# Kernel tuning notes

Hardware: AMD Instinct MI355X
Metric: run time of the kernel (lower is better)

Reference implementation:

```python
import jax, jax.numpy as jnp
import numpy as np

N_HEADS = 8
HEAD_DIM = 64  # hidden_dim 512 / 8 heads
EPS = 1e-12    # F.normalize clamp_min eps


def setup_inputs() -> dict:
    key = jax.random.key(0)
    k1, k2, k3, k4 = jax.random.split(key, 4)
    B, C, H, W = 2, 256, 48, 48
    hidden = N_HEADS * HEAD_DIM
    x = jax.random.normal(k1, (B, C, H, W), dtype=jnp.float32)
    w_qkv = jax.random.normal(k2, (hidden * 3, C), dtype=jnp.float32) * 0.02
    w_proj = jax.random.normal(k3, (C, hidden), dtype=jnp.float32) * 0.02
    b_proj = jax.random.normal(k4, (C,), dtype=jnp.float32) * 0.02
    return {"x": x, "w_qkv": w_qkv, "w_proj": w_proj, "b_proj": b_proj}


def _l2norm_tokens(t):
    # normalize along the token axis (last dim), matching F.normalize(dim=-1)
    n = jnp.sqrt(jnp.sum(t * t, axis=-1, keepdims=True))
    return t / jnp.maximum(n, EPS)


def reference(x, w_qkv, w_proj, b_proj):
    B, C, H, W = x.shape
    N = H * W
    # 1x1 conv == channel matmul
    qkv = jnp.einsum('oc,bchw->bohw', w_qkv, x)  # [B, 3*hidden, H, W]
    qkv = qkv.reshape(B, 3, N_HEADS, HEAD_DIM, N)
    q, k, v = qkv[:, 0], qkv[:, 1], qkv[:, 2]    # each [B, h, d, N]
    q = _l2norm_tokens(q)
    k = _l2norm_tokens(k)
    # attn = q^T @ k over head_dim -> [B, h, N, N]; note: qk_scale unused in source
    attn = jnp.einsum('bhdn,bhdm->bhnm', q, k)
    attn = jax.nn.softmax(attn, axis=-1)
    # out = attn @ v^T -> [B, h, N, d], then permute to [B, h, d, N]
    out = jnp.einsum('bhnm,bhdm->bhdn', attn, v)
    out = out.reshape(B, N_HEADS * HEAD_DIM, H, W)
    # proj 1x1 conv with bias
    y = jnp.einsum('oc,bchw->bohw', w_proj, out) + b_proj[None, :, None, None]
    return y
```

## Files before the change

kernel.cpp:

```cpp
#include <hip/hip_runtime.h>
#include <math.h>

#define NTOK 2304
#define BATCH 2
#define CIN 256
#define HID 512
#define NH 8
#define LOG2E 1.44269504088896340736f

typedef __attribute__((ext_vector_type(8))) short bfrag;
typedef __attribute__((ext_vector_type(16))) float f32x16;

#if __has_builtin(__builtin_amdgcn_exp2f)
#define EXP2(x) __builtin_amdgcn_exp2f(x)
#else
#define EXP2(x) exp2f(x)
#endif

__device__ __forceinline__ unsigned f2bf(float f) {
    unsigned u = __float_as_uint(f);
    u += 0x7FFF + ((u >> 16) & 1);
    return u >> 16;
}

__device__ __forceinline__ unsigned pk_trunc(float a, float b) {
    return __builtin_amdgcn_perm(__float_as_uint(b), __float_as_uint(a), 0x07060302u);
}

__device__ __forceinline__ void softmax_frag(
    const f32x16& accS, int h, float& ps0, float& ps1, bfrag& P0, bfrag& P1)
{
    unsigned dw[8];
#pragma unroll
    for (int i = 0; i < 8; i++) {
        float plo = EXP2(accS[2 * i]);
        float phi = EXP2(accS[2 * i + 1]);
        dw[i] = pk_trunc(plo, phi);
        ps0 += __uint_as_float(dw[i] << 16);
        ps1 += __uint_as_float(dw[i] & 0xffff0000u);
    }
    unsigned sa0 = h ? dw[0] : dw[2], sb0 = h ? dw[1] : dw[3];
    unsigned sa1 = h ? dw[4] : dw[6], sb1 = h ? dw[5] : dw[7];
    unsigned ra0 = (unsigned)__shfl_xor((int)sa0, 32, 64);
    unsigned rb0 = (unsigned)__shfl_xor((int)sb0, 32, 64);
    unsigned ra1 = (unsigned)__shfl_xor((int)sa1, 32, 64);
    unsigned rb1 = (unsigned)__shfl_xor((int)sb1, 32, 64);
    union { bfrag f; unsigned u[4]; } U0, U1;
    U0.u[0] = h ? ra0 : dw[0];  U0.u[1] = h ? rb0 : dw[1];
    U0.u[2] = h ? dw[2] : ra0;  U0.u[3] = h ? dw[3] : rb0;
    U1.u[0] = h ? ra1 : dw[4];  U1.u[1] = h ? rb1 : dw[5];
    U1.u[2] = h ? dw[6] : ra1;  U1.u[3] = h ? dw[7] : rb1;
    P0 = U0.f; P1 = U1.f;
}

__global__ __launch_bounds__(256) void pack_weights(
    const float* __restrict__ wq, short* __restrict__ wqb,
    const float* __restrict__ wp, short* __restrict__ wpb)
{
    int e = (blockIdx.x * 256 + threadIdx.x) * 8;
    const int NQ = 1536 * 256;
    const float* src; short* dst;
    if (e < NQ) {
        int row = e >> 8, c = e & 255;
        int off = (((row >> 5) * 16 + (c >> 4)) * 64 + ((c >> 3) & 1) * 32 + (row & 31)) * 8;
        src = wq + e; dst = wqb + off;
    } else {
        int e2 = e - NQ;
        int row = e2 >> 9, c = e2 & 511;
        int off = (((row >> 5) * 32 + (c >> 4)) * 64 + ((c >> 3) & 1) * 32 + (row & 31)) * 8;
        src = wp + e2; dst = wpb + off;
    }
    float4 v0 = ((const float4*)src)[0];
    float4 v1 = ((const float4*)src)[1];
    unsigned b0 = f2bf(v0.x) | (f2bf(v0.y) << 16);
    unsigned b1 = f2bf(v0.z) | (f2bf(v0.w) << 16);
    unsigned b2 = f2bf(v1.x) | (f2bf(v1.y) << 16);
    unsigned b3 = f2bf(v1.z) | (f2bf(v1.w) << 16);
    *((uint4*)dst) = make_uint4(b0, b1, b2, b3);
}

__global__ __launch_bounds__(256) void pack_xT(
    const float* __restrict__ x, short* __restrict__ xT)
{
    int n0 = blockIdx.x * 64, c0 = blockIdx.y * 64, b = blockIdx.z;
    __shared__ float sT[64][65];
    int tid = threadIdx.x, lane = tid & 63, wv = tid >> 6;
    for (int c = wv; c < 64; c += 4)
        sT[c][lane] = x[((size_t)b * CIN + c0 + c) * NTOK + n0 + lane];
    __syncthreads();
    int n = tid >> 2, c4 = (tid & 3) * 16;
    unsigned buf[8];
#pragma unroll
    for (int i = 0; i < 8; i++)
        buf[i] = f2bf(sT[c4 + 2 * i][n]) | (f2bf(sT[c4 + 2 * i + 1][n]) << 16);
    int n_tok = n0 + n;
    int l31n = n & 31;
    short* dst = xT + (((size_t)b * 72 + (n_tok >> 5)) * 16 + ((c0 + c4) >> 4)) * 512;
    ((uint4*)(dst + (0 * 32 + l31n) * 8))[0] = make_uint4(buf[0], buf[1], buf[2], buf[3]);
    ((uint4*)(dst + (1 * 32 + l31n) * 8))[0] = make_uint4(buf[4], buf[5], buf[6], buf[7]);
}

__global__ __launch_bounds__(256, 2) void gemm_qkv(
    const short* __restrict__ A,
    const short* __restrict__ B,
    float* __restrict__ qkf, short* __restrict__ vb)
{
    int b = blockIdx.z;
    int o0 = blockIdx.y * 128;
    int n0 = blockIdx.x * 128;
    int tid = threadIdx.x, wv = tid >> 6, lane = tid & 63;
    int h = lane >> 5, l31 = lane & 31;

    const short* pa = A + ((size_t)(o0 >> 5) * 16) * 512 + lane * 8;
    const short* pb = B + (((size_t)b * 72 + (n0 >> 5) + wv) * 16) * 512 + lane * 8;

    f32x16 acc[4];
#pragma unroll
    for (int rb = 0; rb < 4; rb++)
#pragma unroll
        for (int r = 0; r < 16; r++) acc[rb][r] = 0.f;

#pragma unroll 2
    for (int kc = 0; kc < 16; kc++) {
        bfrag a0 = *(const bfrag*)(pa + (size_t)(0 * 16 + kc) * 512);
        bfrag a1 = *(const bfrag*)(pa + (size_t)(1 * 16 + kc) * 512);
        bfrag a2 = *(const bfrag*)(pa + (size_t)(2 * 16 + kc) * 512);
        bfrag a3 = *(const bfrag*)(pa + (size_t)(3 * 16 + kc) * 512);
        bfrag bb = *(const bfrag*)(pb + (size_t)kc * 512);
        acc[0] = __builtin_amdgcn_mfma_f32_32x32x16_bf16(a0, bb, acc[0], 0, 0, 0);
        acc[1] = __builtin_amdgcn_mfma_f32_32x32x16_bf16(a1, bb, acc[1], 0, 0, 0);
        acc[2] = __builtin_amdgcn_mfma_f32_32x32x16_bf16(a2, bb, acc[2], 0, 0, 0);
        acc[3] = __builtin_amdgcn_mfma_f32_32x32x16_bf16(a3, bb, acc[3], 0, 0, 0);
    }

    int nn = n0 + wv * 32 + l31;
    if (o0 < 1024) {
        float* Q = qkf + (size_t)b * 1024 * NTOK;
#pragma unroll
        for (int rb = 0; rb < 4; rb++)
#pragma unroll
            for (int r = 0; r < 16; r++) {
                int ml = (r & 3) + 8 * (r >> 2) + 4 * h;
                Q[(size_t)(o0 + rb * 32 + ml) * NTOK + nn] = acc[rb][r];
            }
    } else {
        short* V = vb + (size_t)b * 512 * NTOK;
        int ov = o0 - 1024;
        int mb = nn >> 5, jc = (nn >> 4) & 1, hv = (nn >> 3) & 1, e = nn & 7;
#pragma unroll
        for (int rb = 0; rb < 4; rb++)
#pragma unroll
            for (int r = 0; r < 16; r++) {
                int ml = (r & 3) + 8 * (r >> 2) + 4 * h;
                int row = ov + rb * 32 + ml;
                int hh2 = row >> 6, dl = row & 63;
                int jr = dl >> 5, l31v = dl & 31;
                V[((((size_t)hh2 * 72 + mb) * 4 + jr * 2 + jc) * 64
                   + hv * 32 + l31v) * 8 + e] = (short)f2bf(acc[rb][r]);
            }
    }
}

__global__ __launch_bounds__(256) void rownorm(
    const float* __restrict__ qkf, float* __restrict__ invn)
{
    int row = blockIdx.x;
    int b = row >> 10, o = row & 1023;
    const float* p = qkf + ((size_t)b * 1024 + o) * NTOK;
    int tid = threadIdx.x;
    float s = 0.f;
    for (int n = tid; n < NTOK; n += 256) { float v = p[n]; s += v * v; }
#pragma unroll
    for (int off = 32; off > 0; off >>= 1) s += __shfl_down(s, off, 64);
    __shared__ float ws[4];
    if ((tid & 63) == 0) ws[tid >> 6] = s;
    __syncthreads();
    if (tid == 0) {
        float tot = ws[0] + ws[1] + ws[2] + ws[3];
        invn[row] = 1.f / fmaxf(sqrtf(tot), 1e-12f);
    }
}

__global__ __launch_bounds__(256) void pack_qk(
    const float* __restrict__ qkf, const float* __restrict__ invn,
    short* __restrict__ qkt)
{
    int n0 = blockIdx.x * 64;
    int bh = blockIdx.y;
    int sel = blockIdx.z;
    int b = bh >> 3, h = bh & 7;
    const float* src = qkf + ((size_t)b * 1024 + sel * 512 + h * 64) * NTOK;
    int base = b * 1024 + sel * 512 + h * 64;
    float extra = sel == 0 ? LOG2E : 1.f;

    __shared__ float sT[64][65];
    int tid = threadIdx.x, lane = tid & 63, wv = tid >> 6;
    for (int d = wv; d < 64; d += 4)
        sT[d][lane] = src[(size_t)d * NTOK + n0 + lane] * (invn[base + d] * extra);
    __syncthreads();

    int n = tid >> 2, c4 = (tid & 3) * 16;
    unsigned buf[8];
#pragma unroll
    for (int i = 0; i < 8; i++)
        buf[i] = f2bf(sT[c4 + 2 * i][n]) | (f2bf(sT[c4 + 2 * i + 1][n]) << 16);
    int t = n0 + n;
    int mb = t >> 5, l31 = t & 31, fi = c4 >> 4;
    short* dst = qkt + (size_t)sel * ((size_t)16 * NTOK * 64)
               + (size_t)bh * NTOK * 64
               + ((size_t)mb * 4 + fi) * 512;
    ((uint4*)(dst + (0 * 32 + l31) * 8))[0] = make_uint4(buf[0], buf[1], buf[2], buf[3]);
    ((uint4*)(dst + (1 * 32 + l31) * 8))[0] = make_uint4(buf[4], buf[5], buf[6], buf[7]);
}

__global__ __launch_bounds__(256, 4) void attn_nb(
    const short* __restrict__ qkt,
    const short* __restrict__ vb,
    short* __restrict__ Opart,
    float* __restrict__ lsum)
{
    int bid = blockIdx.x;
    int g = bid & 63;
    int bh = g >> 2, ms = g & 3;
    int ntile = bid >> 6;
    int b = bh >> 3, hh = bh & 7;
    int tid = threadIdx.x, wv = tid >> 6, lane = tid & 63;
    int h = lane >> 5, l31 = lane & 31;
    int nb = ntile * 128 + wv * 32;
    int mb0 = ms * 18;

    const short* Qt = qkt + (size_t)bh * NTOK * 64;
    const short* kp = qkt + (size_t)16 * NTOK * 64 + (size_t)bh * NTOK * 64
                    + ((size_t)mb0 * 4) * 512 + lane * 8;
    const short* vp = vb + (((size_t)(b * 8 + hh) * 72 + mb0) * 4) * 512 + lane * 8;

    bfrag bQ[4];
    {
        const short* q0 = Qt + ((size_t)(nb >> 5) * 4) * 512 + lane * 8;
#pragma unroll
        for (int i = 0; i < 4; i++) bQ[i] = *(const bfrag*)(q0 + i * 512);
    }

    f32x16 aL, aH;
#pragma unroll
    for (int r = 0; r < 16; r++) { aL[r] = 0.f; aH[r] = 0.f; }
    float s0 = 0.f, s1 = 0.f;

    bfrag ck[4], cv[4];
#pragma unroll
    for (int i = 0; i < 4; i++) {
        ck[i] = *(const bfrag*)(kp + i * 512);
        cv[i] = *(const bfrag*)(vp + i * 512);
    }

#pragma unroll 2
    for (int it = 0; it < 18; it++) {
        kp += 2048; vp += 2048;
        bfrag nk[4], nv[4];
#pragma unroll
        for (int i = 0; i < 4; i++) {
            nk[i] = *(const bfrag*)(kp + i * 512);
            nv[i] = *(const bfrag*)(vp + i * 512);
        }

        bfrag P0, P1;
        {
            f32x16 accS;
#pragma unroll
            for (int r = 0; r < 16; r++) accS[r] = 0.f;
            accS = __builtin_amdgcn_mfma_f32_32x32x16_bf16(ck[0], bQ[0], accS, 0, 0, 0);
            accS = __builtin_amdgcn_mfma_f32_32x32x16_bf16(ck[1], bQ[1], accS, 0, 0, 0);
            accS = __builtin_amdgcn_mfma_f32_32x32x16_bf16(ck[2], bQ[2], accS, 0, 0, 0);
            accS = __builtin_amdgcn_mfma_f32_32x32x16_bf16(ck[3], bQ[3], accS, 0, 0, 0);
            softmax_frag(accS, h, s0, s1, P0, P1);
        }
        aL = __builtin_amdgcn_mfma_f32_32x32x16_bf16(P0, cv[0], aL, 0, 0, 0);
        aL = __builtin_amdgcn_mfma_f32_32x32x16_bf16(P1, cv[1], aL, 0, 0, 0);
        aH = __builtin_amdgcn_mfma_f32_32x32x16_bf16(P0, cv[2], aH, 0, 0, 0);
        aH = __builtin_amdgcn_mfma_f32_32x32x16_bf16(P1, cv[3], aH, 0, 0, 0);

#pragma unroll
        for (int i = 0; i < 4; i++) { ck[i] = nk[i]; cv[i] = nv[i]; }
    }

    float p0 = s0 + s1;
    p0 += __shfl_xor(p0, 32, 64);
    if (h == 0)
        lsum[((size_t)ms * 16 + bh) * NTOK + nb + l31] = p0;

    short* Ob = Opart + (size_t)ms * (2ull * NTOK * HID)
              + (size_t)b * NTOK * HID + hh * 64;
#pragma unroll
    for (int r = 0; r < 16; r++) {
        int ml = (r & 3) + 8 * (r >> 2) + 4 * h;
        Ob[(size_t)(nb + ml) * HID + l31] = (short)f2bf(aL[r]);
        Ob[(size_t)(nb + ml) * HID + 32 + l31] = (short)f2bf(aH[r]);
    }
}

__global__ __launch_bounds__(256) void combine(
    const short* __restrict__ Opart, const float* __restrict__ lsum,
    short* __restrict__ aoT)
{
    int s = blockIdx.x * 256 + threadIdx.x;
    int lane = s & 63, kc = (s >> 6) & 31, nbb = s >> 11;
    int b = nbb >= 72 ? 1 : 0, nb = nbb - 72 * b;
    int h = lane >> 5, l31 = lane & 31;
    int n = nb * 32 + l31;
    int k0 = kc * 16 + h * 8;
    int hh = kc >> 2;
    float l = 0.f;
#pragma unroll
    for (int ms = 0; ms < 4; ms++)
        l += lsum[((size_t)ms * 16 + b * 8 + hh) * NTOK + n];
    float inv = 1.f / l;
    float a[8] = {0.f, 0.f, 0.f, 0.f, 0.f, 0.f, 0.f, 0.f};
#pragma unroll
    for (int ms = 0; ms < 4; ms++) {
        const short* P = Opart + (size_t)ms * (2ull * NTOK * HID)
                       + ((size_t)b * NTOK + n) * HID + k0;
        uint4 v = *(const uint4*)P;
        a[0] += __uint_as_float(v.x << 16);
        a[1] += __uint_as_float(v.x & 0xffff0000u);
        a[2] += __uint_as_float(v.y << 16);
        a[3] += __uint_as_float(v.y & 0xffff0000u);
        a[4] += __uint_as_float(v.z << 16);
        a[5] += __uint_as_float(v.z & 0xffff0000u);
        a[6] += __uint_as_float(v.w << 16);
        a[7] += __uint_as_float(v.w & 0xffff0000u);
    }
    unsigned b0 = f2bf(a[0] * inv) | (f2bf(a[1] * inv) << 16);
    unsigned b1 = f2bf(a[2] * inv) | (f2bf(a[3] * inv) << 16);
    unsigned b2 = f2bf(a[4] * inv) | (f2bf(a[5] * inv) << 16);
    unsigned b3 = f2bf(a[6] * inv) | (f2bf(a[7] * inv) << 16);
    *((uint4*)(aoT + (size_t)s * 8)) = make_uint4(b0, b1, b2, b3);
}

__global__ __launch_bounds__(256, 2) void gemm_proj(
    const short* __restrict__ A,
    const short* __restrict__ B,
    const float* __restrict__ bias, float* __restrict__ y)
{
    int b = blockIdx.z;
    int o0 = blockIdx.y * 64;
    int n0 = blockIdx.x * 128;
    int tid = threadIdx.x, wv = tid >> 6, lane = tid & 63;
    int h = lane >> 5, l31 = lane & 31;

    const short* pa = A + ((size_t)(o0 >> 5) * 32) * 512 + lane * 8;
    const short* pb = B + (((size_t)b * 72 + (n0 >> 5) + wv) * 32) * 512 + lane * 8;

    f32x16 acc0, acc1;
#pragma unroll
    for (int r = 0; r < 16; r++) { acc0[r] = 0.f; acc1[r] = 0.f; }

#pragma unroll 4
    for (int kc = 0; kc < 32; kc++) {
        bfrag a0 = *(const bfrag*)(pa + (size_t)kc * 512);
        bfrag a1 = *(const bfrag*)(pa + (size_t)(32 + kc) * 512);
        bfrag bb = *(const bfrag*)(pb + (size_t)kc * 512);
        acc0 = __builtin_amdgcn_mfma_f32_32x32x16_bf16(a0, bb, acc0, 0, 0, 0);
        acc1 = __builtin_amdgcn_mfma_f32_32x32x16_bf16(a1, bb, acc1, 0, 0, 0);
    }

    int nn = n0 + wv * 32 + l31;
#pragma unroll
    for (int r = 0; r < 16; r++) {
        int ml = (r & 3) + 8 * (r >> 2) + 4 * h;
        y[((size_t)b * CIN + o0 + ml) * NTOK + nn] = acc0[r] + bias[o0 + ml];
        y[((size_t)b * CIN + o0 + 32 + ml) * NTOK + nn] = acc1[r] + bias[o0 + 32 + ml];
    }
}

extern "C" void kernel_launch(void* const* d_in, const int* in_sizes, int n_in,
                              void* d_out, int out_size, void* d_ws, size_t ws_size,
                              hipStream_t stream)
{
    const float* x      = (const float*)d_in[0];
    const float* w_qkv  = (const float*)d_in[1];
    const float* w_proj = (const float*)d_in[2];
    const float* b_proj = (const float*)d_in[3];
    float* y = (float*)d_out;

    float* qkf   = (float*)d_ws;
    short* Opart = (short*)d_ws;
    short* vb    = (short*)((char*)d_ws + 18874368);
    short* qkt   = (short*)((char*)d_ws + 23592960);
    short* aoT   = (short*)((char*)d_ws + 23592960);
    float* lsum  = (float*)((char*)d_ws + 33030144);
    short* xT    = (short*)((char*)d_ws + 33030144);
    short* wqb   = (short*)((char*)d_ws + 35389440);
    short* wpb   = (short*)((char*)d_ws + 36175872);
    float* invn  = (float*)((char*)d_ws + 36438016);

    pack_weights<<<(1536 * 256 + 256 * 512) / 8 / 256, 256, 0, stream>>>(
        w_qkv, wqb, w_proj, wpb);
    pack_xT<<<dim3(NTOK / 64, CIN / 64, BATCH), 256, 0, stream>>>(x, xT);
    gemm_qkv<<<dim3(NTOK / 128, 1536 / 128, BATCH), 256, 0, stream>>>(
        wqb, xT, qkf, vb);
    rownorm<<<2048, 256, 0, stream>>>(qkf, invn);
    pack_qk<<<dim3(NTOK / 64, BATCH * NH, 2), 256, 0, stream>>>(qkf, invn, qkt);
    attn_nb<<<1152, 256, 0, stream>>>(qkt, vb, Opart, lsum);
    combine<<<1152, 256, 0, stream>>>(Opart, lsum, aoT);
    gemm_proj<<<dim3(NTOK / 128, CIN / 64, BATCH), 256, 0, stream>>>(
        wpb, aoT, b_proj, y);
}
```

Before: 144.1 us.

## Process two query tiles per wave in attention to reuse K/V fragments

Each wave of the attention kernel now handles two 32-token query tiles (nb0 and nb0+64) while sharing the same loaded K and V fragments. Blocks shrink to 128 threads, so the same 1152-block grid still covers every 128-token tile. This halves K/V global loads per query and gives more independent MFMA work to interleave, at the cost of roughly doubled accumulator registers and lower occupancy (launch bounds 128,2). The softmax row-sum accumulation is also rewritten as a tree reduction to shorten the dependency chain.

```diff
diff --git a/kernel.cpp b/kernel.cpp
--- a/kernel.cpp
+++ b/kernel.cpp
@@ -31,14 +31,17 @@
     const f32x16& accS, int h, float& ps0, float& ps1, bfrag& P0, bfrag& P1)
 {
     unsigned dw[8];
+    float e0[8], e1[8];
 #pragma unroll
     for (int i = 0; i < 8; i++) {
         float plo = EXP2(accS[2 * i]);
         float phi = EXP2(accS[2 * i + 1]);
         dw[i] = pk_trunc(plo, phi);
-        ps0 += __uint_as_float(dw[i] << 16);
-        ps1 += __uint_as_float(dw[i] & 0xffff0000u);
-    }
+        e0[i] = __uint_as_float(dw[i] << 16);
+        e1[i] = __uint_as_float(dw[i] & 0xffff0000u);
+    }
+    ps0 += ((e0[0] + e0[1]) + (e0[2] + e0[3])) + ((e0[4] + e0[5]) + (e0[6] + e0[7]));
+    ps1 += ((e1[0] + e1[1]) + (e1[2] + e1[3])) + ((e1[4] + e1[5]) + (e1[6] + e1[7]));
     unsigned sa0 = h ? dw[0] : dw[2], sb0 = h ? dw[1] : dw[3];
     unsigned sa1 = h ? dw[4] : dw[6], sb1 = h ? dw[5] : dw[7];
     unsigned ra0 = (unsigned)__shfl_xor((int)sa0, 32, 64);
@@ -213,7 +216,7 @@
     ((uint4*)(dst + (1 * 32 + l31) * 8))[0] = make_uint4(buf[4], buf[5], buf[6], buf[7]);
 }
 
-__global__ __launch_bounds__(256, 4) void attn_nb(
+__global__ __launch_bounds__(128, 2) void attn_nb(
     const short* __restrict__ qkt,
     const short* __restrict__ vb,
     short* __restrict__ Opart,
@@ -226,7 +229,8 @@
     int b = bh >> 3, hh = bh & 7;
     int tid = threadIdx.x, wv = tid >> 6, lane = tid & 63;
     int h = lane >> 5, l31 = lane & 31;
-    int nb = ntile * 128 + wv * 32;
+    int nb0 = ntile * 128 + wv * 32;
+    int nb1 = nb0 + 64;
     int mb0 = ms * 18;
 
     const short* Qt = qkt + (size_t)bh * NTOK * 64;
@@ -234,17 +238,21 @@
                     + ((size_t)mb0 * 4) * 512 + lane * 8;
     const short* vp = vb + (((size_t)(b * 8 + hh) * 72 + mb0) * 4) * 512 + lane * 8;
 
-    bfrag bQ[4];
+    bfrag bQ0[4], bQ1[4];
     {
-        const short* q0 = Qt + ((size_t)(nb >> 5) * 4) * 512 + lane * 8;
-#pragma unroll
-        for (int i = 0; i < 4; i++) bQ[i] = *(const bfrag*)(q0 + i * 512);
-    }
-
-    f32x16 aL, aH;
-#pragma unroll
-    for (int r = 0; r < 16; r++) { aL[r] = 0.f; aH[r] = 0.f; }
-    float s0 = 0.f, s1 = 0.f;
+        const short* q0 = Qt + ((size_t)(nb0 >> 5) * 4) * 512 + lane * 8;
+        const short* q1 = Qt + ((size_t)(nb1 >> 5) * 4) * 512 + lane * 8;
+#pragma unroll
+        for (int i = 0; i < 4; i++) {
+            bQ0[i] = *(const bfrag*)(q0 + i * 512);
+            bQ1[i] = *(const bfrag*)(q1 + i * 512);
+        }
+    }
+
+    f32x16 aL0, aH0, aL1, aH1;
+#pragma unroll
+    for (int r = 0; r < 16; r++) { aL0[r] = 0.f; aH0[r] = 0.f; aL1[r] = 0.f; aH1[r] = 0.f; }
+    float s00 = 0.f, s01 = 0.f, s10 = 0.f, s11 = 0.f;
 
     bfrag ck[4], cv[4];
 #pragma unroll
@@ -263,38 +271,58 @@
             nv[i] = *(const bfrag*)(vp + i * 512);
         }
 
-        bfrag P0, P1;
+        bfrag P00, P01, P10, P11;
         {
             f32x16 accS;
 #pragma unroll
             for (int r = 0; r < 16; r++) accS[r] = 0.f;
-            accS = __builtin_amdgcn_mfma_f32_32x32x16_bf16(ck[0], bQ[0], accS, 0, 0, 0);
-            accS = __builtin_amdgcn_mfma_f32_32x32x16_bf16(ck[1], bQ[1], accS, 0, 0, 0);
-            accS = __builtin_amdgcn_mfma_f32_32x32x16_bf16(ck[2], bQ[2], accS, 0, 0, 0);
-            accS = __builtin_amdgcn_mfma_f32_32x32x16_bf16(ck[3], bQ[3], accS, 0, 0, 0);
-            softmax_frag(accS, h, s0, s1, P0, P1);
+            accS = __builtin_amdgcn_mfma_f32_32x32x16_bf16(ck[0], bQ0[0], accS, 0, 0, 0);
+            accS = __builtin_amdgcn_mfma_f32_32x32x16_bf16(ck[1], bQ0[1], accS, 0, 0, 0);
+            accS = __builtin_amdgcn_mfma_f32_32x32x16_bf16(ck[2], bQ0[2], accS, 0, 0, 0);
+            accS = __builtin_amdgcn_mfma_f32_32x32x16_bf16(ck[3], bQ0[3], accS, 0, 0, 0);
+            softmax_frag(accS, h, s00, s01, P00, P01);
         }
-        aL = __builtin_amdgcn_mfma_f32_32x32x16_bf16(P0, cv[0], aL, 0, 0, 0);
-        aL = __builtin_amdgcn_mfma_f32_32x32x16_bf16(P1, cv[1], aL, 0, 0, 0);
-        aH = __builtin_amdgcn_mfma_f32_32x32x16_bf16(P0, cv[2], aH, 0, 0, 0);
-        aH = __builtin_amdgcn_mfma_f32_32x32x16_bf16(P1, cv[3], aH, 0, 0, 0);
+        {
+            f32x16 accS;
+#pragma unroll
+            for (int r = 0; r < 16; r++) accS[r] = 0.f;
+            accS = __builtin_amdgcn_mfma_f32_32x32x16_bf16(ck[0], bQ1[0], accS, 0, 0, 0);
+            accS = __builtin_amdgcn_mfma_f32_32x32x16_bf16(ck[1], bQ1[1], accS, 0, 0, 0);
+            accS = __builtin_amdgcn_mfma_f32_32x32x16_bf16(ck[2], bQ1[2], accS, 0, 0, 0);
+            accS = __builtin_amdgcn_mfma_f32_32x32x16_bf16(ck[3], bQ1[3], accS, 0, 0, 0);
+            softmax_frag(accS, h, s10, s11, P10, P11);
+        }
+        aL0 = __builtin_amdgcn_mfma_f32_32x32x16_bf16(P00, cv[0], aL0, 0, 0, 0);
+        aL0 = __builtin_amdgcn_mfma_f32_32x32x16_bf16(P01, cv[1], aL0, 0, 0, 0);
+        aH0 = __builtin_amdgcn_mfma_f32_32x32x16_bf16(P00, cv[2], aH0, 0, 0, 0);
+        aH0 = __builtin_amdgcn_mfma_f32_32x32x16_bf16(P01, cv[3], aH0, 0, 0, 0);
+        aL1 = __builtin_amdgcn_mfma_f32_32x32x16_bf16(P10, cv[0], aL1, 0, 0, 0);
+        aL1 = __builtin_amdgcn_mfma_f32_32x32x16_bf16(P11, cv[1], aL1, 0, 0, 0);
+        aH1 = __builtin_amdgcn_mfma_f32_32x32x16_bf16(P10, cv[2], aH1, 0, 0, 0);
+        aH1 = __builtin_amdgcn_mfma_f32_32x32x16_bf16(P11, cv[3], aH1, 0, 0, 0);
 
 #pragma unroll
         for (int i = 0; i < 4; i++) { ck[i] = nk[i]; cv[i] = nv[i]; }
     }
 
-    float p0 = s0 + s1;
+    float p0 = s00 + s01;
     p0 += __shfl_xor(p0, 32, 64);
-    if (h == 0)
-        lsum[((size_t)ms * 16 + bh) * NTOK + nb + l31] = p0;
+    float p1 = s10 + s11;
+    p1 += __shfl_xor(p1, 32, 64);
+    if (h == 0) {
+        lsum[((size_t)ms * 16 + bh) * NTOK + nb0 + l31] = p0;
+        lsum[((size_t)ms * 16 + bh) * NTOK + nb1 + l31] = p1;
+    }
 
     short* Ob = Opart + (size_t)ms * (2ull * NTOK * HID)
               + (size_t)b * NTOK * HID + hh * 64;
 #pragma unroll
     for (int r = 0; r < 16; r++) {
         int ml = (r & 3) + 8 * (r >> 2) + 4 * h;
-        Ob[(size_t)(nb + ml) * HID + l31] = (short)f2bf(aL[r]);
-        Ob[(size_t)(nb + ml) * HID + 32 + l31] = (short)f2bf(aH[r]);
+        Ob[(size_t)(nb0 + ml) * HID + l31] = (short)f2bf(aL0[r]);
+        Ob[(size_t)(nb0 + ml) * HID + 32 + l31] = (short)f2bf(aH0[r]);
+        Ob[(size_t)(nb1 + ml) * HID + l31] = (short)f2bf(aL1[r]);
+        Ob[(size_t)(nb1 + ml) * HID + 32 + l31] = (short)f2bf(aH1[r]);
     }
 }
 
@@ -400,7 +428,7 @@
         wqb, xT, qkf, vb);
     rownorm<<<2048, 256, 0, stream>>>(qkf, invn);
     pack_qk<<<dim3(NTOK / 64, BATCH * NH, 2), 256, 0, stream>>>(qkf, invn, qkt);
-    attn_nb<<<1152, 256, 0, stream>>>(qkt, vb, Opart, lsum);
+    attn_nb<<<1152, 128, 0, stream>>>(qkt, vb, Opart, lsum);
     combine<<<1152, 256, 0, stream>>>(Opart, lsum, aoT);
     gemm_proj<<<dim3(NTOK / 128, CIN / 64, BATCH), 256, 0, stream>>>(
         wpb, aoT, b_proj, y);
```

Result: no change. 144.1 us (+0.0%).
